# Optimization experiments

Hardware: AMD Instinct MI355X
Metric: run time of the kernel (lower is better)

Reference implementation:

```python
import jax, jax.numpy as jnp
import numpy as np

NUM_CAPSULE = 16
DIM_CAPSULE = 16
NUM_ROUTING = 3
EPS = 1e-7  # K.epsilon()


def squash(v, axis=-1):
    s2 = jnp.sum(jnp.square(v), axis=axis, keepdims=True) + EPS
    scale = s2 / ((1.0 + s2) * jnp.sqrt(s2))
    return scale * v


def setup_inputs() -> dict:
    key = jax.random.key(0)
    k1, k2 = jax.random.split(key)
    B, N, IC, ID = 64, 128, 32, 8
    x = jax.random.normal(k1, (B, N, IC, ID), dtype=jnp.float32)
    # glorot_uniform for W: [IC, ID, NUM_CAPSULE*DIM_CAPSULE]
    fan_in, fan_out = ID, NUM_CAPSULE * DIM_CAPSULE
    limit = np.sqrt(6.0 / (fan_in + fan_out))
    W = jax.random.uniform(k2, (IC, ID, NUM_CAPSULE * DIM_CAPSULE), dtype=jnp.float32,
                           minval=-limit, maxval=limit)
    return {"x": x, "W": W}


def reference(x, W):
    B, N, IC, ID = x.shape
    NC, DC = NUM_CAPSULE, DIM_CAPSULE
    u = x.reshape(-1, IC, ID)  # [BN, IC, ID]
    # prediction vectors: [BN, IC, NC*DC] -> [BN, NC, IC, DC]
    u_hat = jnp.einsum('bij,ijk->bik', u, W).reshape(-1, IC, NC, DC).transpose(0, 2, 1, 3)
    u_hat_stopped = jax.lax.stop_gradient(u_hat)
    b = jnp.zeros((u_hat.shape[0], NC, IC), dtype=x.dtype)
    outputs = None
    for i in range(NUM_ROUTING):
        c = jax.nn.softmax(b, axis=1)  # softmax over num_capsule axis (dim=1 in source)
        hat = u_hat if i == NUM_ROUTING - 1 else u_hat_stopped
        outputs = squash(jnp.einsum('bci,bcid->bcd', c, hat))  # [BN, NC, DC]
        if i < NUM_ROUTING - 1:
            b = b + jnp.einsum('bcd,bcid->bci', outputs, u_hat_stopped)
    return outputs.reshape(B, N, NC, DC)
```

## Files before the change

kernel.cpp:

```cpp
#include <hip/hip_runtime.h>
#include <hip/hip_bf16.h>


#define S 2

typedef float    v2f __attribute__((ext_vector_type(2)));
typedef _Float16 v2h __attribute__((ext_vector_type(2)));

__device__ __forceinline__ v2h pack2h(float a, float b) {
  return __builtin_bit_cast(v2h, __builtin_amdgcn_cvt_pkrtz(a, b));
}

template <int CTRL>
__device__ __forceinline__ float dppf(float x) {
  return __builtin_bit_cast(float,
      __builtin_amdgcn_update_dpp(0, __builtin_bit_cast(int, x), CTRL, 0xF, 0xF, true));
}
template <int CTRL>
__device__ __forceinline__ v2h dpph(v2h v) {
  return __builtin_bit_cast(v2h,
      __builtin_amdgcn_update_dpp(0, __builtin_bit_cast(int, v), CTRL, 0xF, 0xF, true));
}
template <int CTRL, int BANK>
__device__ __forceinline__ int dpp_old_i(int old, int x) {
  return __builtin_amdgcn_update_dpp(old, x, CTRL, 0xF, BANK, false);
}
__device__ __forceinline__ v2h xor4t_h(v2h s) {
  int si = __builtin_bit_cast(int, s);
  int ya = dpp_old_i<0x104, 0x5>(0, si);
  return __builtin_bit_cast(v2h, dpp_old_i<0x114, 0xA>(ya, si));
}

#if __has_builtin(__builtin_amdgcn_fdot2)
__device__ __forceinline__ float dot2(v2h a, v2h b, float c) {
  return __builtin_amdgcn_fdot2(a, b, c, false);
}
#else
__device__ __forceinline__ float dot2(v2h a, v2h b, float c) {
  return fmaf((float)a.x, (float)b.x, fmaf((float)a.y, (float)b.y, c));
}
#endif

__global__ __launch_bounds__(256) void prep_kernel(const float* __restrict__ W,
                                                   const float* __restrict__ x,
                                                   _Float16* __restrict__ Wth,
                                                   _Float16* __restrict__ xh) {
  int bid = blockIdx.x;
  if (bid < 256) {
    int o  = bid * 256 + threadIdx.x;
    int ic = o >> 11;
    int k  = (o >> 3) & 255;
    int id = o & 7;
    Wth[o] = (_Float16)W[(ic * 8 + id) * 256 + k];
  } else {
    int tid = (bid - 256) * 256 + threadIdx.x;
    const float4* xp = (const float4*)x + tid * 2;
    float4 f0 = xp[0], f1 = xp[1];
    v2h h0 = {(_Float16)f0.x, (_Float16)f0.y};
    v2h h1 = {(_Float16)f0.z, (_Float16)f0.w};
    v2h h2 = {(_Float16)f1.x, (_Float16)f1.y};
    v2h h3 = {(_Float16)f1.z, (_Float16)f1.w};
    uint4 o;
    o.x = __builtin_bit_cast(unsigned, h0);
    o.y = __builtin_bit_cast(unsigned, h1);
    o.z = __builtin_bit_cast(unsigned, h2);
    o.w = __builtin_bit_cast(unsigned, h3);
    ((uint4*)xh)[tid] = o;
  }
}

__device__ __forceinline__ v2f squash2(v2f o) {
  v2f s2 = o * o;
  s2.x += dppf<0xB1>(s2.x);   s2.y += dppf<0xB1>(s2.y);
  s2.x += dppf<0x4E>(s2.x);   s2.y += dppf<0x4E>(s2.y);
  s2.x += dppf<0x141>(s2.x);  s2.y += dppf<0x141>(s2.y);
  s2.x += dppf<0x140>(s2.x);  s2.y += dppf<0x140>(s2.y);
  s2 += (v2f){1e-7f, 1e-7f};
  v2f sc;
  sc.x = s2.x * __builtin_amdgcn_rsqf(s2.x) * __builtin_amdgcn_rcpf(1.f + s2.x);
  sc.y = s2.y * __builtin_amdgcn_rsqf(s2.y) * __builtin_amdgcn_rcpf(1.f + s2.y);
  return o * sc;
}

template <bool ASSIGN>
__device__ __forceinline__ void b_update2(v2h vh, const v2h* uh, int dc,
                                          float* bp0, float* bp1) {
#pragma unroll
  for (int icb = 0; icb < 32; icb += 16) {
    v2h a[16];
#pragma unroll
    for (int j = 0; j < 16; ++j) a[j] = vh * uh[icb + j];
    v2h b8[8];
    const bool u8 = (dc & 8) != 0;
#pragma unroll
    for (int j = 0; j < 8; ++j) {
      v2h send = u8 ? a[j] : a[j + 8];
      v2h recv = dpph<0x128>(send);
      b8[j] = (u8 ? a[j + 8] : a[j]) + recv;
    }
    v2h c4[4];
    const bool u4 = (dc & 4) != 0;
#pragma unroll
    for (int j = 0; j < 4; ++j) {
      v2h send = u4 ? b8[j] : b8[j + 4];
      v2h recv = xor4t_h(send);
      c4[j] = (u4 ? b8[j + 4] : b8[j]) + recv;
    }
    v2h d2[2];
    const bool u2 = (dc & 2) != 0;
#pragma unroll
    for (int j = 0; j < 2; ++j) {
      v2h send = u2 ? c4[j] : c4[j + 2];
      v2h recv = dpph<0x4E>(send);
      d2[j] = (u2 ? c4[j + 2] : c4[j]) + recv;
    }
    const bool u1 = (dc & 1) != 0;
    v2h send = u1 ? d2[0] : d2[1];
    v2h recv = dpph<0xB1>(send);
    v2h e = (u1 ? d2[1] : d2[0]) + recv;
    float e0 = (float)e.x, e1 = (float)e.y;
    if (ASSIGN) { bp0[icb + dc] = e0;  bp1[icb + dc] = e1; }
    else        { bp0[icb + dc] += e0; bp1[icb + dc] += e1; }
  }
}

#define CSTRIDE 40

__global__ __launch_bounds__(256, 6) void caps_kernel(const _Float16* __restrict__ xh,
                                                      const uint4* __restrict__ Wt4,
                                                      float* __restrict__ out) {
  const int t  = threadIdx.x;
  const int nc = t >> 4;
  const int dc = t & 15;
  const int s0 = blockIdx.x * S;

  __shared__ float b_lds[S][16][33];
  __shared__ v2h c16h[16 * CSTRIDE];

  v2h uh[32];
  v2f o2 = (v2f){0.f, 0.f};

  const v2h* xp0 = (const v2h*)(xh + (s0 + 0) * 256);
  const v2h* xp1 = (const v2h*)(xh + (s0 + 1) * 256);
#pragma unroll
  for (int ic = 0; ic < 32; ++ic) {
    uint4 wv = Wt4[ic * 256 + t];
    v2h w0 = __builtin_bit_cast(v2h, wv.x);
    v2h w1 = __builtin_bit_cast(v2h, wv.y);
    v2h w2 = __builtin_bit_cast(v2h, wv.z);
    v2h w3 = __builtin_bit_cast(v2h, wv.w);
    float a0 = dot2(xp0[ic * 4 + 3], w3,
               dot2(xp0[ic * 4 + 2], w2,
               dot2(xp0[ic * 4 + 1], w1,
               dot2(xp0[ic * 4 + 0], w0, 0.f))));
    float a1 = dot2(xp1[ic * 4 + 3], w3,
               dot2(xp1[ic * 4 + 2], w2,
               dot2(xp1[ic * 4 + 1], w1,
               dot2(xp1[ic * 4 + 0], w0, 0.f))));
    o2 += (v2f){a0, a1};
    uh[ic] = pack2h(a0, a1);
  }

  {
    v2f v = squash2(o2 * (v2f){0.0625f, 0.0625f});
    v2h vh = pack2h(v.x, v.y);
    b_update2<true>(vh, uh, dc, &b_lds[0][nc][0], &b_lds[1][nc][0]);
  }
  __syncthreads();

#pragma unroll
  for (int r = 1; r < 3; ++r) {
    {
      const int ss  = t >> 7;
      const int icc = (t >> 2) & 31;
      const int q   = t & 3;
      float e0 = __expf(b_lds[ss][4 * q + 0][icc]);
      float e1 = __expf(b_lds[ss][4 * q + 1][icc]);
      float e2 = __expf(b_lds[ss][4 * q + 2][icc]);
      float e3 = __expf(b_lds[ss][4 * q + 3][icc]);
      float ps = (e0 + e1) + (e2 + e3);
      ps += dppf<0xB1>(ps);
      ps += dppf<0x4E>(ps);
      float inv = __builtin_amdgcn_rcpf(ps);
      _Float16* cw = (_Float16*)c16h + ss;
      cw[((4 * q + 0) * CSTRIDE + icc) * 2] = (_Float16)(e0 * inv);
      cw[((4 * q + 1) * CSTRIDE + icc) * 2] = (_Float16)(e1 * inv);
      cw[((4 * q + 2) * CSTRIDE + icc) * 2] = (_Float16)(e2 * inv);
      cw[((4 * q + 3) * CSTRIDE + icc) * 2] = (_Float16)(e3 * inv);
    }
    __syncthreads();

    const v2h* crow = &c16h[nc * CSTRIDE];
    v2h oh = (v2h){(_Float16)0.f, (_Float16)0.f};
#pragma unroll
    for (int j = 0; j < 16; ++j) {
      v2h cA = crow[j];
      v2h cB = crow[j + 16];
      oh = __builtin_elementwise_fma(cA, uh[j], oh);
      oh = __builtin_elementwise_fma(cB, uh[16 + j], oh);
    }
    v2f o = (v2f){(float)oh.x, (float)oh.y};
    v2f v = squash2(o);
    if (r == 2) {
      out[(s0 + 0) * 256 + t] = v.x;
      out[(s0 + 1) * 256 + t] = v.y;
    } else {
      v2h vh = pack2h(v.x, v.y);
      b_update2<false>(vh, uh, dc, &b_lds[0][nc][0], &b_lds[1][nc][0]);
      __syncthreads();
    }
  }
}

extern "C" void kernel_launch(void* const* d_in, const int* in_sizes, int n_in,
                              void* d_out, int out_size, void* d_ws, size_t ws_size,
                              hipStream_t stream) {
  const float* x = (const float*)d_in[0];
  const float* W = (const float*)d_in[1];
  _Float16* Wth = (_Float16*)d_ws;
  _Float16* xh  = (_Float16*)d_ws + 65536;

  prep_kernel<<<1280, 256, 0, stream>>>(W, x, Wth, xh);
  caps_kernel<<<8192 / S, 256, 0, stream>>>(xh, (const uint4*)Wth, (float*)d_out);
}
```

Before: 91.30 us.

## Process four samples per block to amortize W loads and sync overhead

New measurement: 96.44 us. 1.06x slower.

```diff
diff --git a/kernel.cpp b/kernel.cpp
--- a/kernel.cpp
+++ b/kernel.cpp
@@ -2,7 +2,7 @@
 #include <hip/hip_bf16.h>
 
 
-#define S 2
+#define S 4
 
 typedef float    v2f __attribute__((ext_vector_type(2)));
 typedef _Float16 v2h __attribute__((ext_vector_type(2)));
@@ -83,50 +83,63 @@
 }
 
 template <bool ASSIGN>
-__device__ __forceinline__ void b_update2(v2h vh, const v2h* uh, int dc,
-                                          float* bp0, float* bp1) {
+__device__ __forceinline__ void b_update4(v2h vh01, v2h vh23,
+                                          const v2h* uh01, const v2h* uh23, int dc,
+                                          float* bp0, float* bp1,
+                                          float* bp2, float* bp3) {
 #pragma unroll
   for (int icb = 0; icb < 32; icb += 16) {
-    v2h a[16];
-#pragma unroll
-    for (int j = 0; j < 16; ++j) a[j] = vh * uh[icb + j];
-    v2h b8[8];
+    v2h a01[16], a23[16];
+#pragma unroll
+    for (int j = 0; j < 16; ++j) {
+      a01[j] = vh01 * uh01[icb + j];
+      a23[j] = vh23 * uh23[icb + j];
+    }
+    v2h b801[8], b823[8];
     const bool u8 = (dc & 8) != 0;
 #pragma unroll
     for (int j = 0; j < 8; ++j) {
-      v2h send = u8 ? a[j] : a[j + 8];
-      v2h recv = dpph<0x128>(send);
-      b8[j] = (u8 ? a[j + 8] : a[j]) + recv;
-    }
-    v2h c4[4];
+      v2h s01 = u8 ? a01[j] : a01[j + 8];
+      v2h s23 = u8 ? a23[j] : a23[j + 8];
+      b801[j] = (u8 ? a01[j + 8] : a01[j]) + dpph<0x128>(s01);
+      b823[j] = (u8 ? a23[j + 8] : a23[j]) + dpph<0x128>(s23);
+    }
+    v2h c401[4], c423[4];
     const bool u4 = (dc & 4) != 0;
 #pragma unroll
     for (int j = 0; j < 4; ++j) {
-      v2h send = u4 ? b8[j] : b8[j + 4];
-      v2h recv = xor4t_h(send);
-      c4[j] = (u4 ? b8[j + 4] : b8[j]) + recv;
-    }
-    v2h d2[2];
+      v2h s01 = u4 ? b801[j] : b801[j + 4];
+      v2h s23 = u4 ? b823[j] : b823[j + 4];
+      c401[j] = (u4 ? b801[j + 4] : b801[j]) + xor4t_h(s01);
+      c423[j] = (u4 ? b823[j + 4] : b823[j]) + xor4t_h(s23);
+    }
+    v2h d201[2], d223[2];
     const bool u2 = (dc & 2) != 0;
 #pragma unroll
     for (int j = 0; j < 2; ++j) {
-      v2h send = u2 ? c4[j] : c4[j + 2];
-      v2h recv = dpph<0x4E>(send);
-      d2[j] = (u2 ? c4[j + 2] : c4[j]) + recv;
+      v2h s01 = u2 ? c401[j] : c401[j + 2];
+      v2h s23 = u2 ? c423[j] : c423[j + 2];
+      d201[j] = (u2 ? c401[j + 2] : c401[j]) + dpph<0x4E>(s01);
+      d223[j] = (u2 ? c423[j + 2] : c423[j]) + dpph<0x4E>(s23);
     }
     const bool u1 = (dc & 1) != 0;
-    v2h send = u1 ? d2[0] : d2[1];
-    v2h recv = dpph<0xB1>(send);
-    v2h e = (u1 ? d2[1] : d2[0]) + recv;
-    float e0 = (float)e.x, e1 = (float)e.y;
-    if (ASSIGN) { bp0[icb + dc] = e0;  bp1[icb + dc] = e1; }
-    else        { bp0[icb + dc] += e0; bp1[icb + dc] += e1; }
-  }
-}
-
-#define CSTRIDE 40
-
-__global__ __launch_bounds__(256, 6) void caps_kernel(const _Float16* __restrict__ xh,
+    v2h s01 = u1 ? d201[0] : d201[1];
+    v2h s23 = u1 ? d223[0] : d223[1];
+    v2h e01 = (u1 ? d201[1] : d201[0]) + dpph<0xB1>(s01);
+    v2h e23 = (u1 ? d223[1] : d223[0]) + dpph<0xB1>(s23);
+    if (ASSIGN) {
+      bp0[icb + dc] = (float)e01.x;  bp1[icb + dc] = (float)e01.y;
+      bp2[icb + dc] = (float)e23.x;  bp3[icb + dc] = (float)e23.y;
+    } else {
+      bp0[icb + dc] += (float)e01.x; bp1[icb + dc] += (float)e01.y;
+      bp2[icb + dc] += (float)e23.x; bp3[icb + dc] += (float)e23.y;
+    }
+  }
+}
+
+#define CSTRIDE 41
+
+__global__ __launch_bounds__(256, 4) void caps_kernel(const _Float16* __restrict__ xh,
                                                       const uint4* __restrict__ Wt4,
                                                       float* __restrict__ out) {
   const int t  = threadIdx.x;
@@ -135,13 +148,16 @@
   const int s0 = blockIdx.x * S;
 
   __shared__ float b_lds[S][16][33];
-  __shared__ v2h c16h[16 * CSTRIDE];
-
-  v2h uh[32];
-  v2f o2 = (v2f){0.f, 0.f};
+  __shared__ v2h c01[16 * CSTRIDE];
+  __shared__ v2h c23[16 * CSTRIDE];
+
+  v2h uh01[32], uh23[32];
+  v2f o01 = (v2f){0.f, 0.f}, o23 = (v2f){0.f, 0.f};
 
   const v2h* xp0 = (const v2h*)(xh + (s0 + 0) * 256);
   const v2h* xp1 = (const v2h*)(xh + (s0 + 1) * 256);
+  const v2h* xp2 = (const v2h*)(xh + (s0 + 2) * 256);
+  const v2h* xp3 = (const v2h*)(xh + (s0 + 3) * 256);
 #pragma unroll
   for (int ic = 0; ic < 32; ++ic) {
     uint4 wv = Wt4[ic * 256 + t];
@@ -149,64 +165,73 @@
     v2h w1 = __builtin_bit_cast(v2h, wv.y);
     v2h w2 = __builtin_bit_cast(v2h, wv.z);
     v2h w3 = __builtin_bit_cast(v2h, wv.w);
-    float a0 = dot2(xp0[ic * 4 + 3], w3,
-               dot2(xp0[ic * 4 + 2], w2,
-               dot2(xp0[ic * 4 + 1], w1,
-               dot2(xp0[ic * 4 + 0], w0, 0.f))));
-    float a1 = dot2(xp1[ic * 4 + 3], w3,
-               dot2(xp1[ic * 4 + 2], w2,
-               dot2(xp1[ic * 4 + 1], w1,
-               dot2(xp1[ic * 4 + 0], w0, 0.f))));
-    o2 += (v2f){a0, a1};
-    uh[ic] = pack2h(a0, a1);
+    float a0 = dot2(xp0[ic * 4 + 3], w3, dot2(xp0[ic * 4 + 2], w2,
+               dot2(xp0[ic * 4 + 1], w1, dot2(xp0[ic * 4 + 0], w0, 0.f))));
+    float a1 = dot2(xp1[ic * 4 + 3], w3, dot2(xp1[ic * 4 + 2], w2,
+               dot2(xp1[ic * 4 + 1], w1, dot2(xp1[ic * 4 + 0], w0, 0.f))));
+    float a2 = dot2(xp2[ic * 4 + 3], w3, dot2(xp2[ic * 4 + 2], w2,
+               dot2(xp2[ic * 4 + 1], w1, dot2(xp2[ic * 4 + 0], w0, 0.f))));
+    float a3 = dot2(xp3[ic * 4 + 3], w3, dot2(xp3[ic * 4 + 2], w2,
+               dot2(xp3[ic * 4 + 1], w1, dot2(xp3[ic * 4 + 0], w0, 0.f))));
+    o01 += (v2f){a0, a1};
+    o23 += (v2f){a2, a3};
+    uh01[ic] = pack2h(a0, a1);
+    uh23[ic] = pack2h(a2, a3);
   }
 
   {
-    v2f v = squash2(o2 * (v2f){0.0625f, 0.0625f});
-    v2h vh = pack2h(v.x, v.y);
-    b_update2<true>(vh, uh, dc, &b_lds[0][nc][0], &b_lds[1][nc][0]);
+    v2f v01 = squash2(o01 * (v2f){0.0625f, 0.0625f});
+    v2f v23 = squash2(o23 * (v2f){0.0625f, 0.0625f});
+    b_update4<true>(pack2h(v01.x, v01.y), pack2h(v23.x, v23.y), uh01, uh23, dc,
+                    &b_lds[0][nc][0], &b_lds[1][nc][0],
+                    &b_lds[2][nc][0], &b_lds[3][nc][0]);
   }
   __syncthreads();
 
 #pragma unroll
   for (int r = 1; r < 3; ++r) {
     {
-      const int ss  = t >> 7;
-      const int icc = (t >> 2) & 31;
-      const int q   = t & 3;
-      float e0 = __expf(b_lds[ss][4 * q + 0][icc]);
-      float e1 = __expf(b_lds[ss][4 * q + 1][icc]);
-      float e2 = __expf(b_lds[ss][4 * q + 2][icc]);
-      float e3 = __expf(b_lds[ss][4 * q + 3][icc]);
-      float ps = (e0 + e1) + (e2 + e3);
-      ps += dppf<0xB1>(ps);
-      ps += dppf<0x4E>(ps);
-      float inv = __builtin_amdgcn_rcpf(ps);
-      _Float16* cw = (_Float16*)c16h + ss;
-      cw[((4 * q + 0) * CSTRIDE + icc) * 2] = (_Float16)(e0 * inv);
-      cw[((4 * q + 1) * CSTRIDE + icc) * 2] = (_Float16)(e1 * inv);
-      cw[((4 * q + 2) * CSTRIDE + icc) * 2] = (_Float16)(e2 * inv);
-      cw[((4 * q + 3) * CSTRIDE + icc) * 2] = (_Float16)(e3 * inv);
+      const int ss  = t >> 6;
+      const int icc = (t >> 1) & 31;
+      const int h   = t & 1;
+      float e[8];
+      float sum = 0.f;
+#pragma unroll
+      for (int n = 0; n < 8; ++n) {
+        e[n] = __expf(b_lds[ss][8 * h + n][icc]);
+        sum += e[n];
+      }
+      sum += dppf<0xB1>(sum);
+      float inv = __builtin_amdgcn_rcpf(sum);
+      _Float16* cw = (_Float16*)(ss < 2 ? c01 : c23) + (ss & 1);
+#pragma unroll
+      for (int n = 0; n < 8; ++n)
+        cw[((8 * h + n) * CSTRIDE + icc) * 2] = (_Float16)(e[n] * inv);
     }
     __syncthreads();
 
-    const v2h* crow = &c16h[nc * CSTRIDE];
-    v2h oh = (v2h){(_Float16)0.f, (_Float16)0.f};
+    const v2h* crow01 = &c01[nc * CSTRIDE];
+    const v2h* crow23 = &c23[nc * CSTRIDE];
+    v2h oh01 = (v2h){(_Float16)0.f, (_Float16)0.f};
+    v2h oh23 = (v2h){(_Float16)0.f, (_Float16)0.f};
 #pragma unroll
     for (int j = 0; j < 16; ++j) {
-      v2h cA = crow[j];
-      v2h cB = crow[j + 16];
-      oh = __builtin_elementwise_fma(cA, uh[j], oh);
-      oh = __builtin_elementwise_fma(cB, uh[16 + j], oh);
-    }
-    v2f o = (v2f){(float)oh.x, (float)oh.y};
-    v2f v = squash2(o);
+      oh01 = __builtin_elementwise_fma(crow01[j],      uh01[j],      oh01);
+      oh01 = __builtin_elementwise_fma(crow01[j + 16], uh01[16 + j], oh01);
+      oh23 = __builtin_elementwise_fma(crow23[j],      uh23[j],      oh23);
+      oh23 = __builtin_elementwise_fma(crow23[j + 16], uh23[16 + j], oh23);
+    }
+    v2f v01 = squash2((v2f){(float)oh01.x, (float)oh01.y});
+    v2f v23 = squash2((v2f){(float)oh23.x, (float)oh23.y});
     if (r == 2) {
-      out[(s0 + 0) * 256 + t] = v.x;
-      out[(s0 + 1) * 256 + t] = v.y;
+      out[(s0 + 0) * 256 + t] = v01.x;
+      out[(s0 + 1) * 256 + t] = v01.y;
+      out[(s0 + 2) * 256 + t] = v23.x;
+      out[(s0 + 3) * 256 + t] = v23.y;
     } else {
-      v2h vh = pack2h(v.x, v.y);
-      b_update2<false>(vh, uh, dc, &b_lds[0][nc][0], &b_lds[1][nc][0]);
+      b_update4<false>(pack2h(v01.x, v01.y), pack2h(v23.x, v23.y), uh01, uh23, dc,
+                       &b_lds[0][nc][0], &b_lds[1][nc][0],
+                       &b_lds[2][nc][0], &b_lds[3][nc][0]);
       __syncthreads();
     }
   }
```
